# Kernel tuning notes

Measured on AMD Instinct MI355X. Metric: run time of the kernel, lower is better.

The kernel has to match this reference:

```python
import jax, jax.numpy as jnp
import numpy as np
import math

DIM = 384
HEADS = 6
HEAD_DIM = DIM // HEADS
MLP_HIDDEN = int(DIM * 2.0)


def layer_norm(x, g, b, eps=1e-5):
    mu = jnp.mean(x, axis=-1, keepdims=True)
    var = jnp.mean((x - mu) ** 2, axis=-1, keepdims=True)
    return (x - mu) * jax.lax.rsqrt(var + eps) * g + b


def setup_inputs() -> dict:
    key = jax.random.key(0)
    ks = jax.random.split(key, 12)
    B, N = 4, 2048
    s = 0.02
    return {
        "x": jax.random.normal(ks[0], (B, N, DIM), dtype=jnp.float32),
        "pos": jax.random.normal(ks[1], (B, N, 3), dtype=jnp.float32),
        "qkv_w": jax.random.normal(ks[2], (DIM, 3 * DIM), dtype=jnp.float32) * s,
        "qkv_b": jnp.zeros((3 * DIM,), jnp.float32),
        "proj_w": jax.random.normal(ks[3], (DIM, DIM), dtype=jnp.float32) * s,
        "proj_b": jnp.zeros((DIM,), jnp.float32),
        "mlp_w1": jax.random.normal(ks[4], (DIM, MLP_HIDDEN), dtype=jnp.float32) * s,
        "mlp_b1": jnp.zeros((MLP_HIDDEN,), jnp.float32),
        "mlp_w2": jax.random.normal(ks[5], (MLP_HIDDEN, DIM), dtype=jnp.float32) * s,
        "mlp_b2": jnp.zeros((DIM,), jnp.float32),
        "ln1_g": jnp.ones((DIM,), jnp.float32),
        "ln1_b": jnp.zeros((DIM,), jnp.float32),
        "ln2_g": jnp.ones((DIM,), jnp.float32),
        "ln2_b": jnp.zeros((DIM,), jnp.float32),
    }


def reference(x, pos, qkv_w, qkv_b, proj_w, proj_b, mlp_w1, mlp_b1,
              mlp_w2, mlp_b2, ln1_g, ln1_b, ln2_g, ln2_b):
    B, N, D = x.shape
    H, Hd = HEADS, HEAD_DIM
    # qkv projection
    qkv = layer_norm(x, ln1_g, ln1_b) @ qkv_w + qkv_b          # [B,N,3D]
    qkv = qkv.reshape(B, N, 3, H, Hd)
    q = jnp.transpose(qkv[:, :, 0], (0, 2, 1, 3))               # [B,H,N,Hd]
    k = jnp.transpose(qkv[:, :, 1], (0, 2, 1, 3))
    v = jnp.transpose(qkv[:, :, 2], (0, 2, 1, 3))
    # pairwise squared-distance bias: exp(-||p_i - p_j||^2)
    rel = pos[:, :, None, :] - pos[:, None, :, :]               # [B,N,N,3]
    dist = jnp.exp(-jnp.sum(rel ** 2, axis=-1))                 # [B,N,N]
    scale = 1.0 / math.sqrt(Hd)
    attn = jnp.einsum('bhqd,bhkd->bhqk', q, k) * scale + dist[:, None, :, :]
    attn = jax.nn.softmax(attn, axis=-1)
    out = jnp.einsum('bhqk,bhkd->bhqd', attn, v)                # [B,H,N,Hd]
    out = jnp.transpose(out, (0, 2, 1, 3)).reshape(B, N, D)
    out = out @ proj_w + proj_b
    x = x + out
    h = layer_norm(x, ln2_g, ln2_b)
    h = jax.nn.gelu(h @ mlp_w1 + mlp_b1, approximate=False) @ mlp_w2 + mlp_b2
    return x + h
```

## Files before the change

### kernel.cpp

```cpp
#include <hip/hip_runtime.h>
#include <hip/hip_bf16.h>
#include <math.h>

#define DIMD 384
#define NHEADS 6
#define HD 64
#define MLPH 768
#define SEQ 2048
#define NBATCH 4
#define NTOK (NBATCH*SEQ)

typedef __hip_bfloat16 bf16;

typedef __attribute__((ext_vector_type(8))) short bf16x8;
typedef __attribute__((ext_vector_type(4))) float f32x4;

#define LOG2E 1.44269504088896340736f

static __device__ inline float fexp2(float x) { return __builtin_amdgcn_exp2f(x); }

static __device__ inline f32x4 mfma16(bf16x8 a, bf16x8 b, f32x4 c) {
    return __builtin_amdgcn_mfma_f32_16x16x32_bf16(a, b, c, 0, 0, 0);
}

static __device__ inline unsigned int cvtpk(float lo, float hi) {
    unsigned int r;
    asm("v_cvt_pk_bf16_f32 %0, %1, %2" : "=v"(r) : "v"(lo), "v"(hi));
    return r;
}
static __device__ inline float bflo(unsigned int u) { return __builtin_bit_cast(float, u << 16); }
static __device__ inline float bfhi(unsigned int u) { return __builtin_bit_cast(float, u & 0xffff0000u); }

static __device__ inline void gld16(const void* g, void* l) {
    __builtin_amdgcn_global_load_lds(
        (const __attribute__((address_space(1))) unsigned int*)g,
        (__attribute__((address_space(3))) unsigned int*)l, 16, 0, 0);
}

__global__ __launch_bounds__(256) void ln_k(const float* __restrict__ x,
                                            const float* __restrict__ gm,
                                            const float* __restrict__ bt,
                                            bf16* __restrict__ out) {
    int row = blockIdx.x * 4 + (threadIdx.x >> 6);
    int l = threadIdx.x & 63;
    const float* xr = x + (size_t)row * DIMD;
    float v[6];
#pragma unroll
    for (int j = 0; j < 6; ++j) v[j] = xr[l + 64 * j];
    float s = 0.f, s2 = 0.f;
#pragma unroll
    for (int j = 0; j < 6; ++j) { s += v[j]; s2 += v[j] * v[j]; }
#pragma unroll
    for (int m = 1; m < 64; m <<= 1) { s += __shfl_xor(s, m); s2 += __shfl_xor(s2, m); }
    float mu = s * (1.f / DIMD);
    float var = s2 * (1.f / DIMD) - mu * mu;
    float rs = rsqrtf(var + 1e-5f);
    bf16* orow = out + (size_t)row * DIMD;
#pragma unroll
    for (int j = 0; j < 6; ++j) {
        int i = l + 64 * j;
        orow[i] = __float2bfloat16((v[j] - mu) * rs * gm[i] + bt[i]);
    }
}

__global__ __launch_bounds__(256) void wtransall_k(const float* __restrict__ w1,
                                                   const float* __restrict__ w2,
                                                   const float* __restrict__ w3,
                                                   const float* __restrict__ w4,
                                                   bf16* __restrict__ o1,
                                                   bf16* __restrict__ o2,
                                                   bf16* __restrict__ o3,
                                                   bf16* __restrict__ o4) {
    __shared__ float t[32][33];
    int id = blockIdx.x;
    const float* W; bf16* O; int K, N;
    if (id < 432)      { W = w1; O = o1; K = 384; N = 1152; }
    else if (id < 576) { W = w2; O = o2; K = 384; N = 384;  id -= 432; }
    else if (id < 864) { W = w3; O = o3; K = 384; N = 768;  id -= 576; }
    else               { W = w4; O = o4; K = 768; N = 384;  id -= 864; }
    int nbx = N >> 5;
    int nb = (id % nbx) * 32, kb = (id / nbx) * 32;
    int tx = threadIdx.x & 31, ty = threadIdx.x >> 5;
#pragma unroll
    for (int i = 0; i < 4; ++i)
        t[ty + 8 * i][tx] = W[(size_t)(kb + ty + 8 * i) * N + nb + tx];
    __syncthreads();
#pragma unroll
    for (int i = 0; i < 4; ++i)
        O[(size_t)(nb + ty + 8 * i) * K + kb + tx] = __float2bfloat16(t[tx][ty + 8 * i]);
}

__global__ __launch_bounds__(256) void vtrans_k(const bf16* __restrict__ v_,
                                                bf16* __restrict__ vT_) {
    const unsigned short* v = (const unsigned short*)v_;
    unsigned short* vT = (unsigned short*)vT_;
    __shared__ unsigned short t[32][33];
    int tx = threadIdx.x & 31, ty = threadIdx.x >> 5;
    int nb = blockIdx.x * 32, db = blockIdx.y * 32;
    int bh = blockIdx.z;
    const unsigned short* src = v + (size_t)bh * SEQ * HD;
#pragma unroll
    for (int i = 0; i < 4; ++i)
        t[ty + 8 * i][tx] = src[(size_t)(nb + ty + 8 * i) * HD + db + tx];
    __syncthreads();
    unsigned short* dst = vT + (size_t)bh * HD * SEQ;
    int pc = 8 * ((tx & 15) >> 2) + 4 * (tx >> 4) + (tx & 3);
#pragma unroll
    for (int i = 0; i < 4; ++i)
        dst[(size_t)(db + ty + 8 * i) * SEQ + nb + pc] = t[tx][ty + 8 * i];
}

__global__ __launch_bounds__(256) void dist_k(const float* __restrict__ pos,
                                              bf16* __restrict__ DP) {
    int blk = blockIdx.x;
    int w = blk & 3, qt = (blk >> 2) & 31, b = blk >> 7;
    int l = threadIdx.x & 63, tt = threadIdx.x >> 6;
    int lq = l & 15, g = l >> 4;
    int q = qt * 64 + w * 16 + lq;
    const float* pq = pos + ((size_t)b * SEQ + q) * 3;
    float px = pq[0], py = pq[1], pz = pq[2];
    const float* posb = pos + (size_t)b * SEQ * 3;
    char* base = (char*)DP + (size_t)blk * 65536;
    for (int j = 0; j < 8; ++j) {
        int t = tt * 8 + j;
#pragma unroll
        for (int m = 0; m < 2; ++m) {
            int k0 = t * 64 + 32 * m + 4 * g;
            float a[24];
            const float* pk = posb + 3 * k0;
            *(f32x4*)&a[0]  = *(const f32x4*)pk;
            *(f32x4*)&a[4]  = *(const f32x4*)(pk + 4);
            *(f32x4*)&a[8]  = *(const f32x4*)(pk + 8);
            const float* pk2 = posb + 3 * (k0 + 16);
            *(f32x4*)&a[12] = *(const f32x4*)pk2;
            *(f32x4*)&a[16] = *(const f32x4*)(pk2 + 4);
            *(f32x4*)&a[20] = *(const f32x4*)(pk2 + 8);
            float o8[8];
#pragma unroll
            for (int r = 0; r < 8; ++r) {
                float dx = px - a[3 * r], dy = py - a[3 * r + 1], dz = pz - a[3 * r + 2];
                o8[r] = fexp2(-LOG2E * (dx * dx + dy * dy + dz * dz)) * LOG2E;
            }
            uint4 o;
            o.x = cvtpk(o8[0], o8[1]); o.y = cvtpk(o8[2], o8[3]);
            o.z = cvtpk(o8[4], o8[5]); o.w = cvtpk(o8[6], o8[7]);
            *(uint4*)(base + ((size_t)t * 2 + m) * 1024 + l * 16) = o;
        }
    }
}

template <int EPI>
__global__ __launch_bounds__(256) void gemm128_k(const bf16* __restrict__ A,
                                                 const bf16* __restrict__ WT,
                                                 const float* __restrict__ bias,
                                                 bf16* __restrict__ ob0,
                                                 bf16* __restrict__ ob1,
                                                 bf16* __restrict__ ob2,
                                                 int K, int Nw) {
    __shared__ __align__(16) char Als[2][8192];
    __shared__ __align__(16) char Bls[2][8192];
    int tid = threadIdx.x;
    int w = tid >> 6, l = tid & 63;
    int c = l & 15, g = l >> 4;
    int wr = w >> 1, wc = w & 1;
    int m0 = blockIdx.y * 128, n0 = blockIdx.x * 128;
    const char* Ag = (const char*)A + (size_t)m0 * K * 2;
    const char* Bg = (const char*)WT + (size_t)n0 * K * 2;
    int K2 = K * 2;

    f32x4 acc[4][4];
#pragma unroll
    for (int mi = 0; mi < 4; ++mi)
#pragma unroll
        for (int ni = 0; ni < 4; ++ni) acc[mi][ni] = (f32x4){0.f, 0.f, 0.f, 0.f};

    auto stage = [&](int t, int bi) {
#pragma unroll
        for (int p = 0; p < 2; ++p) {
            int chunk = p * 256 + tid;
            int r = chunk >> 2;
            int cc = ((chunk & 3) ^ (r & 3)) << 4;
            gld16(Ag + (size_t)r * K2 + t * 64 + cc, &Als[bi][chunk * 16]);
            gld16(Bg + (size_t)r * K2 + t * 64 + cc, &Bls[bi][chunk * 16]);
        }
    };

    stage(0, 0);
    int kcn = K >> 5;
    for (int t = 0; t < kcn; ++t) {
        int bi = t & 1;
        __syncthreads();
        if (t + 1 < kcn) stage(t + 1, bi ^ 1);
        bf16x8 af[4], bfr[4];
#pragma unroll
        for (int mi = 0; mi < 4; ++mi) {
            int row = wr * 64 + mi * 16 + c;
            __builtin_memcpy(&af[mi], &Als[bi][row * 64 + ((g ^ (row & 3)) << 4)], 16);
        }
#pragma unroll
        for (int ni = 0; ni < 4; ++ni) {
            int row = wc * 64 + ni * 16 + c;
            __builtin_memcpy(&bfr[ni], &Bls[bi][row * 64 + ((g ^ (row & 3)) << 4)], 16);
        }
#pragma unroll
        for (int mi = 0; mi < 4; ++mi)
#pragma unroll
            for (int ni = 0; ni < 4; ++ni)
                acc[mi][ni] = mfma16(af[mi], bfr[ni], acc[mi][ni]);
    }

#pragma unroll
    for (int mi = 0; mi < 4; ++mi) {
#pragma unroll
        for (int ni = 0; ni < 4; ++ni) {
            int ntb = n0 + wc * 64 + ni * 16;
#pragma unroll
            for (int r = 0; r < 4; ++r) {
                int m = m0 + wr * 64 + mi * 16 + 4 * g + r;
                int n = ntb + c;
                float val = acc[mi][ni][r] + bias[n];
                if (EPI == 0) {
                    int which = ntb / DIMD;
                    int rem = ntb - which * DIMD;
                    int h = rem >> 6;
                    int d = (rem & 63) + c;
                    int b = m >> 11, s = m & (SEQ - 1);
                    bf16* dp = which == 0 ? ob0 : (which == 1 ? ob1 : ob2);
                    dp[(((size_t)b * NHEADS + h) * SEQ + s) * HD + d] = __float2bfloat16(val);
                } else {
                    float ge = 0.5f * val * (1.0f + erff(val * 0.70710678118654752f));
                    ob0[(size_t)m * Nw + n] = __float2bfloat16(ge);
                }
            }
        }
    }
}

template <int EPI>
__global__ __launch_bounds__(256) void gemm_k(const bf16* __restrict__ A,
                                              const bf16* __restrict__ WT,
                                              const float* __restrict__ bias,
                                              const float* __restrict__ resid,
                                              float* __restrict__ outf,
                                              int K, int Nw) {
    __shared__ __align__(16) char Als[2][8192];
    __shared__ __align__(16) char Bls[2][8192];
    int tid = threadIdx.x;
    int w = tid >> 6, l = tid & 63;
    int c = l & 15, g = l >> 4;
    int m0 = blockIdx.y * 64, n0 = blockIdx.x * 64;
    const char* Ag = (const char*)A + (size_t)m0 * K * 2;
    const char* Bg = (const char*)WT + (size_t)n0 * K * 2;
    int K2 = K * 2;

    f32x4 acc[4];
#pragma unroll
    for (int nt = 0; nt < 4; ++nt) acc[nt] = (f32x4){0.f, 0.f, 0.f, 0.f};

    auto stage = [&](int t, int bi) {
#pragma unroll
        for (int p = 0; p < 2; ++p) {
            int chunk = p * 256 + tid;
            int r = chunk >> 3;
            int cc = ((chunk & 7) ^ (r & 7)) << 4;
            gld16(Ag + (size_t)r * K2 + t * 128 + cc, &Als[bi][chunk * 16]);
            gld16(Bg + (size_t)r * K2 + t * 128 + cc, &Bls[bi][chunk * 16]);
        }
    };

    stage(0, 0);
    int kcn = K >> 6;
    int arow = (16 * w + c) * 128;
    int sw = c & 7;
    for (int t = 0; t < kcn; ++t) {
        int bi = t & 1;
        __syncthreads();
        if (t + 1 < kcn) stage(t + 1, bi ^ 1);
#pragma unroll
        for (int kk = 0; kk < 2; ++kk) {
            int ch = ((kk * 4 + g) ^ sw) << 4;
            bf16x8 af;
            __builtin_memcpy(&af, &Als[bi][arow + ch], 16);
#pragma unroll
            for (int nt = 0; nt < 4; ++nt) {
                bf16x8 bfr;
                __builtin_memcpy(&bfr, &Bls[bi][(nt * 16 + c) * 128 + ch], 16);
                acc[nt] = mfma16(af, bfr, acc[nt]);
            }
        }
    }

#pragma unroll
    for (int nt = 0; nt < 4; ++nt) {
        int ntb = n0 + nt * 16;
#pragma unroll
        for (int r = 0; r < 4; ++r) {
            int m = m0 + 16 * w + 4 * g + r;
            int n = ntb + c;
            float val = acc[nt][r] + bias[n];
            val += resid[(size_t)m * Nw + n];
            outf[(size_t)m * Nw + n] = val;
        }
    }
}

__global__ __launch_bounds__(256) void attn_k(const bf16* __restrict__ q,
                                              const bf16* __restrict__ k,
                                              const bf16* __restrict__ vT,
                                              const bf16* __restrict__ DP,
                                              bf16* __restrict__ out) {
    __shared__ __align__(16) char Kls[2][8192];
    __shared__ __align__(16) char Vls[2][8192];

    int tid = threadIdx.x;
    int w = tid >> 6, l = tid & 63;
    int lq = l & 15, g = l >> 4;
    int qt = blockIdx.x & 31;
    int bh = blockIdx.x >> 5;
    int b = bh / NHEADS, h = bh % NHEADS;
    int qrow = qt * 64 + w * 16 + lq;

    const bf16* qp = q + ((size_t)bh * SEQ + qrow) * HD + 8 * g;
    bf16x8 qf0 = *(const bf16x8*)qp;
    bf16x8 qf1 = *(const bf16x8*)(qp + 32);

    const char* kgb = (const char*)(k + (size_t)bh * SEQ * HD);
    const char* vgb = (const char*)(vT + (size_t)bh * HD * SEQ);
    const char* dpb = (const char*)DP + ((size_t)((b * 32 + qt) * 4 + w)) * 65536 + l * 16;

    const float SC2 = 0.125f * LOG2E;
    float lloc = 0.f;
    f32x4 oacc[4];
#pragma unroll
    for (int dt = 0; dt < 4; ++dt) oacc[dt] = (f32x4){0.f, 0.f, 0.f, 0.f};

    auto stage = [&](int t, int bi) {
#pragma unroll
        for (int p = 0; p < 2; ++p) {
            int chunk = p * 256 + tid;
            int r = chunk >> 3, c = chunk & 7;
            int cc = (c ^ (r & 7)) << 4;
            gld16(kgb + (size_t)t * 8192 + r * 128 + cc, &Kls[bi][chunk * 16]);
            gld16(vgb + (size_t)r * 4096 + t * 128 + cc, &Vls[bi][chunk * 16]);
        }
    };

    stage(0, 0);
    uint4 cdp0 = *(const uint4*)(dpb);
    uint4 cdp1 = *(const uint4*)(dpb + 1024);

    int swq = lq & 7;
    for (int t = 0; t < 32; ++t) {
        int bi = t & 1;
        __syncthreads();
        uint4 ndp0 = {0, 0, 0, 0}, ndp1 = {0, 0, 0, 0};
        if (t + 1 < 32) {
            stage(t + 1, bi ^ 1);
            const char* dpn = dpb + (size_t)(t + 1) * 2048;
            ndp0 = *(const uint4*)(dpn);
            ndp1 = *(const uint4*)(dpn + 1024);
        }

        f32x4 st[4];
#pragma unroll
        for (int s = 0; s < 4; ++s) {
            int ro = (16 * s + lq) * 128;
            bf16x8 klo, khi;
            __builtin_memcpy(&klo, &Kls[bi][ro + ((g ^ swq) << 4)], 16);
            __builtin_memcpy(&khi, &Kls[bi][ro + (((4 + g) ^ swq) << 4)], 16);
            f32x4 z = (f32x4){0.f, 0.f, 0.f, 0.f};
            st[s] = mfma16(klo, qf0, z);
            st[s] = mfma16(khi, qf1, st[s]);
        }

#pragma unroll
        for (int m = 0; m < 2; ++m) {
            uint4 cd = m == 0 ? cdp0 : cdp1;
            f32x4 s0v = st[2 * m], s1v = st[2 * m + 1];
            float p[8];
            p[0] = fexp2(s0v[0] * SC2 + bflo(cd.x));
            p[1] = fexp2(s0v[1] * SC2 + bfhi(cd.x));
            p[2] = fexp2(s0v[2] * SC2 + bflo(cd.y));
            p[3] = fexp2(s0v[3] * SC2 + bfhi(cd.y));
            p[4] = fexp2(s1v[0] * SC2 + bflo(cd.z));
            p[5] = fexp2(s1v[1] * SC2 + bfhi(cd.z));
            p[6] = fexp2(s1v[2] * SC2 + bflo(cd.w));
            p[7] = fexp2(s1v[3] * SC2 + bfhi(cd.w));
#pragma unroll
            for (int i = 0; i < 8; ++i) lloc += p[i];

            unsigned int pw[4];
            pw[0] = cvtpk(p[0], p[1]);
            pw[1] = cvtpk(p[2], p[3]);
            pw[2] = cvtpk(p[4], p[5]);
            pw[3] = cvtpk(p[6], p[7]);
            bf16x8 pf;
            __builtin_memcpy(&pf, pw, 16);

#pragma unroll
            for (int dt = 0; dt < 4; ++dt) {
                int rv = (16 * dt + lq) * 128;
                bf16x8 vf;
                __builtin_memcpy(&vf, &Vls[bi][rv + (((4 * m + g) ^ swq) << 4)], 16);
                oacc[dt] = mfma16(vf, pf, oacc[dt]);
            }
        }
        cdp0 = ndp0; cdp1 = ndp1;
    }

    float lrun = lloc;
    lrun += __shfl_xor(lrun, 16);
    lrun += __shfl_xor(lrun, 32);
    float inv = 1.f / lrun;
    bf16* op = out + ((size_t)b * SEQ + qrow) * DIMD + h * HD + 4 * g;
#pragma unroll
    for (int dt = 0; dt < 4; ++dt) {
        unsigned int t2[2];
        t2[0] = cvtpk(oacc[dt][0] * inv, oacc[dt][1] * inv);
        t2[1] = cvtpk(oacc[dt][2] * inv, oacc[dt][3] * inv);
        __builtin_memcpy(op + dt * 16, t2, 8);
    }
}

extern "C" void kernel_launch(void* const* d_in, const int* in_sizes, int n_in,
                              void* d_out, int out_size, void* d_ws, size_t ws_size,
                              hipStream_t stream) {
    const float* x      = (const float*)d_in[0];
    const float* pos    = (const float*)d_in[1];
    const float* qkv_w  = (const float*)d_in[2];
    const float* qkv_b  = (const float*)d_in[3];
    const float* proj_w = (const float*)d_in[4];
    const float* proj_b = (const float*)d_in[5];
    const float* mlp_w1 = (const float*)d_in[6];
    const float* mlp_b1 = (const float*)d_in[7];
    const float* mlp_w2 = (const float*)d_in[8];
    const float* mlp_b2 = (const float*)d_in[9];
    const float* ln1_g  = (const float*)d_in[10];
    const float* ln1_b  = (const float*)d_in[11];
    const float* ln2_g  = (const float*)d_in[12];
    const float* ln2_b  = (const float*)d_in[13];

    char* p = (char*)d_ws;
    size_t off = 0;
    auto alloc = [&](size_t bytes) {
        char* r = p + off;
        off = (off + bytes + 255) & ~(size_t)255;
        return r;
    };
    bf16* WT1 = (bf16*)alloc((size_t)1152 * 384 * 2);
    bf16* WT2 = (bf16*)alloc((size_t)384 * 384 * 2);
    bf16* WT3 = (bf16*)alloc((size_t)384 * 768 * 2);
    bf16* WT4 = (bf16*)alloc((size_t)768 * 384 * 2);
    bf16* xn  = (bf16*)alloc((size_t)NTOK * DIMD * 2);
    bf16* xn2 = (bf16*)alloc((size_t)NTOK * DIMD * 2);
    bf16* qb  = (bf16*)alloc((size_t)NTOK * DIMD * 2);
    bf16* kb  = (bf16*)alloc((size_t)NTOK * DIMD * 2);
    bf16* vb  = (bf16*)alloc((size_t)NTOK * DIMD * 2);
    bf16* vTb = (bf16*)alloc((size_t)NTOK * DIMD * 2);
    bf16* ao  = (bf16*)alloc((size_t)NTOK * DIMD * 2);
    float* x1 = (float*)alloc((size_t)NTOK * DIMD * 4);
    bf16* hh  = (bf16*)alloc((size_t)NTOK * MLPH * 2);
    bf16* dtab = (bf16*)alloc((size_t)NBATCH * SEQ * SEQ * 2);
    if (off > ws_size) return;

    wtransall_k<<<1152, 256, 0, stream>>>(qkv_w, proj_w, mlp_w1, mlp_w2,
                                          WT1, WT2, WT3, WT4);

    dist_k<<<NBATCH * 32 * 4, 256, 0, stream>>>(pos, dtab);

    ln_k<<<NTOK / 4, 256, 0, stream>>>(x, ln1_g, ln1_b, xn);
    gemm128_k<0><<<dim3(1152 / 128, NTOK / 128), 256, 0, stream>>>(
        xn, WT1, qkv_b, qb, kb, vb, 384, 1152);
    vtrans_k<<<dim3(SEQ / 32, HD / 32, NBATCH * NHEADS), 256, 0, stream>>>(vb, vTb);
    attn_k<<<NBATCH * NHEADS * (SEQ / 64), 256, 0, stream>>>(qb, kb, vTb, dtab, ao);
    gemm_k<1><<<dim3(384 / 64, NTOK / 64), 256, 0, stream>>>(
        ao, WT2, proj_b, x, x1, 384, 384);
    ln_k<<<NTOK / 4, 256, 0, stream>>>(x1, ln2_g, ln2_b, xn2);
    gemm128_k<2><<<dim3(768 / 128, NTOK / 128), 256, 0, stream>>>(
        xn2, WT3, mlp_b1, hh, nullptr, nullptr, 384, 768);
    gemm_k<3><<<dim3(384 / 64, NTOK / 64), 256, 0, stream>>>(
        hh, WT4, mlp_b2, x1, (float*)d_out, 768, 384);
}
```

Measured before the change: 144.3 us.

## Merge prep kernels, fuse V transpose into QKV GEMM, triple-buffer attention loop

Combines weight transpose, distance-table generation and the first layernorm into one prep kernel, which removes two launches. The QKV GEMM epilogue now writes V directly in the permuted transposed layout, so the separate V-transpose kernel and its buffer are gone. The attention loop moves from double to triple buffering, using explicit waitcnt, barriers and priority hints. It also computes the softmax row sum with an MFMA against a ones vector in place of per-lane adds and shuffles. This uses more LDS per block, which may lower occupancy, and the epilogue writes to V are scattered.

```diff
diff --git a/kernel.cpp b/kernel.cpp
--- a/kernel.cpp
+++ b/kernel.cpp
@@ -63,88 +63,94 @@
     }
 }
 
-__global__ __launch_bounds__(256) void wtransall_k(const float* __restrict__ w1,
-                                                   const float* __restrict__ w2,
-                                                   const float* __restrict__ w3,
-                                                   const float* __restrict__ w4,
-                                                   bf16* __restrict__ o1,
-                                                   bf16* __restrict__ o2,
-                                                   bf16* __restrict__ o3,
-                                                   bf16* __restrict__ o4) {
+__global__ __launch_bounds__(256) void prep_k(const float* __restrict__ w1,
+                                              const float* __restrict__ w2,
+                                              const float* __restrict__ w3,
+                                              const float* __restrict__ w4,
+                                              bf16* __restrict__ o1,
+                                              bf16* __restrict__ o2,
+                                              bf16* __restrict__ o3,
+                                              bf16* __restrict__ o4,
+                                              const float* __restrict__ pos,
+                                              bf16* __restrict__ DP,
+                                              const float* __restrict__ x,
+                                              const float* __restrict__ g1,
+                                              const float* __restrict__ b1,
+                                              bf16* __restrict__ xn) {
     __shared__ float t[32][33];
     int id = blockIdx.x;
-    const float* W; bf16* O; int K, N;
-    if (id < 432)      { W = w1; O = o1; K = 384; N = 1152; }
-    else if (id < 576) { W = w2; O = o2; K = 384; N = 384;  id -= 432; }
-    else if (id < 864) { W = w3; O = o3; K = 384; N = 768;  id -= 576; }
-    else               { W = w4; O = o4; K = 768; N = 384;  id -= 864; }
-    int nbx = N >> 5;
-    int nb = (id % nbx) * 32, kb = (id / nbx) * 32;
-    int tx = threadIdx.x & 31, ty = threadIdx.x >> 5;
-#pragma unroll
-    for (int i = 0; i < 4; ++i)
-        t[ty + 8 * i][tx] = W[(size_t)(kb + ty + 8 * i) * N + nb + tx];
-    __syncthreads();
-#pragma unroll
-    for (int i = 0; i < 4; ++i)
-        O[(size_t)(nb + ty + 8 * i) * K + kb + tx] = __float2bfloat16(t[tx][ty + 8 * i]);
-}
-
-__global__ __launch_bounds__(256) void vtrans_k(const bf16* __restrict__ v_,
-                                                bf16* __restrict__ vT_) {
-    const unsigned short* v = (const unsigned short*)v_;
-    unsigned short* vT = (unsigned short*)vT_;
-    __shared__ unsigned short t[32][33];
-    int tx = threadIdx.x & 31, ty = threadIdx.x >> 5;
-    int nb = blockIdx.x * 32, db = blockIdx.y * 32;
-    int bh = blockIdx.z;
-    const unsigned short* src = v + (size_t)bh * SEQ * HD;
-#pragma unroll
-    for (int i = 0; i < 4; ++i)
-        t[ty + 8 * i][tx] = src[(size_t)(nb + ty + 8 * i) * HD + db + tx];
-    __syncthreads();
-    unsigned short* dst = vT + (size_t)bh * HD * SEQ;
-    int pc = 8 * ((tx & 15) >> 2) + 4 * (tx >> 4) + (tx & 3);
-#pragma unroll
-    for (int i = 0; i < 4; ++i)
-        dst[(size_t)(db + ty + 8 * i) * SEQ + nb + pc] = t[tx][ty + 8 * i];
-}
-
-__global__ __launch_bounds__(256) void dist_k(const float* __restrict__ pos,
-                                              bf16* __restrict__ DP) {
-    int blk = blockIdx.x;
-    int w = blk & 3, qt = (blk >> 2) & 31, b = blk >> 7;
-    int l = threadIdx.x & 63, tt = threadIdx.x >> 6;
-    int lq = l & 15, g = l >> 4;
-    int q = qt * 64 + w * 16 + lq;
-    const float* pq = pos + ((size_t)b * SEQ + q) * 3;
-    float px = pq[0], py = pq[1], pz = pq[2];
-    const float* posb = pos + (size_t)b * SEQ * 3;
-    char* base = (char*)DP + (size_t)blk * 65536;
-    for (int j = 0; j < 8; ++j) {
-        int t = tt * 8 + j;
-#pragma unroll
-        for (int m = 0; m < 2; ++m) {
-            int k0 = t * 64 + 32 * m + 4 * g;
-            float a[24];
-            const float* pk = posb + 3 * k0;
-            *(f32x4*)&a[0]  = *(const f32x4*)pk;
-            *(f32x4*)&a[4]  = *(const f32x4*)(pk + 4);
-            *(f32x4*)&a[8]  = *(const f32x4*)(pk + 8);
-            const float* pk2 = posb + 3 * (k0 + 16);
-            *(f32x4*)&a[12] = *(const f32x4*)pk2;
-            *(f32x4*)&a[16] = *(const f32x4*)(pk2 + 4);
-            *(f32x4*)&a[20] = *(const f32x4*)(pk2 + 8);
-            float o8[8];
-#pragma unroll
-            for (int r = 0; r < 8; ++r) {
-                float dx = px - a[3 * r], dy = py - a[3 * r + 1], dz = pz - a[3 * r + 2];
-                o8[r] = fexp2(-LOG2E * (dx * dx + dy * dy + dz * dz)) * LOG2E;
+    if (id < 1152) {
+        const float* W; bf16* O; int K, N;
+        if (id < 432)      { W = w1; O = o1; K = 384; N = 1152; }
+        else if (id < 576) { W = w2; O = o2; K = 384; N = 384;  id -= 432; }
+        else if (id < 864) { W = w3; O = o3; K = 384; N = 768;  id -= 576; }
+        else               { W = w4; O = o4; K = 768; N = 384;  id -= 864; }
+        int nbx = N >> 5;
+        int nb = (id % nbx) * 32, kb = (id / nbx) * 32;
+        int tx = threadIdx.x & 31, ty = threadIdx.x >> 5;
+#pragma unroll
+        for (int i = 0; i < 4; ++i)
+            t[ty + 8 * i][tx] = W[(size_t)(kb + ty + 8 * i) * N + nb + tx];
+        __syncthreads();
+#pragma unroll
+        for (int i = 0; i < 4; ++i)
+            O[(size_t)(nb + ty + 8 * i) * K + kb + tx] = __float2bfloat16(t[tx][ty + 8 * i]);
+    } else if (id < 1664) {
+        int blk = id - 1152;
+        int w = blk & 3, qt = (blk >> 2) & 31, b = blk >> 7;
+        int l = threadIdx.x & 63, tt = threadIdx.x >> 6;
+        int lq = l & 15, g = l >> 4;
+        int q = qt * 64 + w * 16 + lq;
+        const float* pq = pos + ((size_t)b * SEQ + q) * 3;
+        float px = pq[0], py = pq[1], pz = pq[2];
+        const float* posb = pos + (size_t)b * SEQ * 3;
+        char* base = (char*)DP + (size_t)blk * 65536;
+        for (int j = 0; j < 8; ++j) {
+            int tt8 = tt * 8 + j;
+#pragma unroll
+            for (int m = 0; m < 2; ++m) {
+                int k0 = tt8 * 64 + 32 * m + 4 * g;
+                float a[24];
+                const float* pk = posb + 3 * k0;
+                *(f32x4*)&a[0]  = *(const f32x4*)pk;
+                *(f32x4*)&a[4]  = *(const f32x4*)(pk + 4);
+                *(f32x4*)&a[8]  = *(const f32x4*)(pk + 8);
+                const float* pk2 = posb + 3 * (k0 + 16);
+                *(f32x4*)&a[12] = *(const f32x4*)pk2;
+                *(f32x4*)&a[16] = *(const f32x4*)(pk2 + 4);
+                *(f32x4*)&a[20] = *(const f32x4*)(pk2 + 8);
+                float o8[8];
+#pragma unroll
+                for (int r = 0; r < 8; ++r) {
+                    float dx = px - a[3 * r], dy = py - a[3 * r + 1], dz = pz - a[3 * r + 2];
+                    o8[r] = fexp2(-LOG2E * (dx * dx + dy * dy + dz * dz)) * LOG2E;
+                }
+                uint4 o;
+                o.x = cvtpk(o8[0], o8[1]); o.y = cvtpk(o8[2], o8[3]);
+                o.z = cvtpk(o8[4], o8[5]); o.w = cvtpk(o8[6], o8[7]);
+                *(uint4*)(base + ((size_t)tt8 * 2 + m) * 1024 + l * 16) = o;
             }
-            uint4 o;
-            o.x = cvtpk(o8[0], o8[1]); o.y = cvtpk(o8[2], o8[3]);
-            o.z = cvtpk(o8[4], o8[5]); o.w = cvtpk(o8[6], o8[7]);
-            *(uint4*)(base + ((size_t)t * 2 + m) * 1024 + l * 16) = o;
+        }
+    } else {
+        int row = (id - 1664) * 4 + (threadIdx.x >> 6);
+        int l = threadIdx.x & 63;
+        const float* xr = x + (size_t)row * DIMD;
+        float v[6];
+#pragma unroll
+        for (int j = 0; j < 6; ++j) v[j] = xr[l + 64 * j];
+        float s = 0.f, s2 = 0.f;
+#pragma unroll
+        for (int j = 0; j < 6; ++j) { s += v[j]; s2 += v[j] * v[j]; }
+#pragma unroll
+        for (int m = 1; m < 64; m <<= 1) { s += __shfl_xor(s, m); s2 += __shfl_xor(s2, m); }
+        float mu = s * (1.f / DIMD);
+        float var = s2 * (1.f / DIMD) - mu * mu;
+        float rs = rsqrtf(var + 1e-5f);
+        bf16* orow = xn + (size_t)row * DIMD;
+#pragma unroll
+        for (int j = 0; j < 6; ++j) {
+            int i = l + 64 * j;
+            orow[i] = __float2bfloat16((v[j] - mu) * rs * g1[i] + b1[i]);
         }
     }
 }
@@ -225,8 +231,13 @@
                     int h = rem >> 6;
                     int d = (rem & 63) + c;
                     int b = m >> 11, s = m & (SEQ - 1);
-                    bf16* dp = which == 0 ? ob0 : (which == 1 ? ob1 : ob2);
-                    dp[(((size_t)b * NHEADS + h) * SEQ + s) * HD + d] = __float2bfloat16(val);
+                    if (which == 2) {
+                        int slot = (s & ~31) + 8 * ((m & 15) >> 2) + 4 * ((m >> 4) & 1) + (m & 3);
+                        ob2[(((size_t)b * NHEADS + h) * HD + d) * SEQ + slot] = __float2bfloat16(val);
+                    } else {
+                        bf16* dp = which == 0 ? ob0 : ob1;
+                        dp[(((size_t)b * NHEADS + h) * SEQ + s) * HD + d] = __float2bfloat16(val);
+                    }
                 } else {
                     float ge = 0.5f * val * (1.0f + erff(val * 0.70710678118654752f));
                     ob0[(size_t)m * Nw + n] = __float2bfloat16(ge);
@@ -309,8 +320,8 @@
                                               const bf16* __restrict__ vT,
                                               const bf16* __restrict__ DP,
                                               bf16* __restrict__ out) {
-    __shared__ __align__(16) char Kls[2][8192];
-    __shared__ __align__(16) char Vls[2][8192];
+    __shared__ __align__(16) char Kls[3][8192];
+    __shared__ __align__(16) char Vls[3][8192];
 
     int tid = threadIdx.x;
     int w = tid >> 6, l = tid & 63;
@@ -329,10 +340,12 @@
     const char* dpb = (const char*)DP + ((size_t)((b * 32 + qt) * 4 + w)) * 65536 + l * 16;
 
     const float SC2 = 0.125f * LOG2E;
-    float lloc = 0.f;
     f32x4 oacc[4];
 #pragma unroll
     for (int dt = 0; dt < 4; ++dt) oacc[dt] = (f32x4){0.f, 0.f, 0.f, 0.f};
+    f32x4 osum = (f32x4){0.f, 0.f, 0.f, 0.f};
+    bf16x8 ones = {(short)0x3F80, (short)0x3F80, (short)0x3F80, (short)0x3F80,
+                   (short)0x3F80, (short)0x3F80, (short)0x3F80, (short)0x3F80};
 
     auto stage = [&](int t, int bi) {
 #pragma unroll
@@ -348,30 +361,29 @@
     stage(0, 0);
     uint4 cdp0 = *(const uint4*)(dpb);
     uint4 cdp1 = *(const uint4*)(dpb + 1024);
-
+    stage(1, 1);
+
+    int ib0 = 0, ib1 = 1, ib2 = 2;
     int swq = lq & 7;
     for (int t = 0; t < 32; ++t) {
-        int bi = t & 1;
-        __syncthreads();
-        uint4 ndp0 = {0, 0, 0, 0}, ndp1 = {0, 0, 0, 0};
-        if (t + 1 < 32) {
-            stage(t + 1, bi ^ 1);
-            const char* dpn = dpb + (size_t)(t + 1) * 2048;
-            ndp0 = *(const uint4*)(dpn);
-            ndp1 = *(const uint4*)(dpn + 1024);
-        }
+        asm volatile("s_waitcnt vmcnt(4)" ::: "memory");
+        __builtin_amdgcn_sched_barrier(0);
+        __builtin_amdgcn_s_barrier();
+        __builtin_amdgcn_sched_barrier(0);
 
         f32x4 st[4];
+        __builtin_amdgcn_s_setprio(1);
 #pragma unroll
         for (int s = 0; s < 4; ++s) {
             int ro = (16 * s + lq) * 128;
             bf16x8 klo, khi;
-            __builtin_memcpy(&klo, &Kls[bi][ro + ((g ^ swq) << 4)], 16);
-            __builtin_memcpy(&khi, &Kls[bi][ro + (((4 + g) ^ swq) << 4)], 16);
+            __builtin_memcpy(&klo, &Kls[ib0][ro + ((g ^ swq) << 4)], 16);
+            __builtin_memcpy(&khi, &Kls[ib0][ro + (((4 + g) ^ swq) << 4)], 16);
             f32x4 z = (f32x4){0.f, 0.f, 0.f, 0.f};
             st[s] = mfma16(klo, qf0, z);
             st[s] = mfma16(khi, qf1, st[s]);
         }
+        __builtin_amdgcn_s_setprio(0);
 
 #pragma unroll
         for (int m = 0; m < 2; ++m) {
@@ -386,8 +398,6 @@
             p[5] = fexp2(s1v[1] * SC2 + bfhi(cd.z));
             p[6] = fexp2(s1v[2] * SC2 + bflo(cd.w));
             p[7] = fexp2(s1v[3] * SC2 + bfhi(cd.w));
-#pragma unroll
-            for (int i = 0; i < 8; ++i) lloc += p[i];
 
             unsigned int pw[4];
             pw[0] = cvtpk(p[0], p[1]);
@@ -397,21 +407,32 @@
             bf16x8 pf;
             __builtin_memcpy(&pf, pw, 16);
 
+            __builtin_amdgcn_s_setprio(1);
+            osum = mfma16(ones, pf, osum);
 #pragma unroll
             for (int dt = 0; dt < 4; ++dt) {
                 int rv = (16 * dt + lq) * 128;
                 bf16x8 vf;
-                __builtin_memcpy(&vf, &Vls[bi][rv + (((4 * m + g) ^ swq) << 4)], 16);
+                __builtin_memcpy(&vf, &Vls[ib0][rv + (((4 * m + g) ^ swq) << 4)], 16);
                 oacc[dt] = mfma16(vf, pf, oacc[dt]);
             }
-        }
+            __builtin_amdgcn_s_setprio(0);
+        }
+
+        __builtin_amdgcn_sched_barrier(0);
+        int tn1 = t + 1 < 32 ? t + 1 : 31;
+        const char* dpn = dpb + (size_t)tn1 * 2048;
+        uint4 ndp0 = *(const uint4*)(dpn);
+        uint4 ndp1 = *(const uint4*)(dpn + 1024);
+        __builtin_amdgcn_sched_barrier(0);
+        int tn2 = t + 2 < 32 ? t + 2 : 31;
+        stage(tn2, ib2);
+        __builtin_amdgcn_sched_barrier(0);
         cdp0 = ndp0; cdp1 = ndp1;
-    }
-
-    float lrun = lloc;
-    lrun += __shfl_xor(lrun, 16);
-    lrun += __shfl_xor(lrun, 32);
-    float inv = 1.f / lrun;
+        int tmp = ib0; ib0 = ib1; ib1 = ib2; ib2 = tmp;
+    }
+
+    float inv = 1.f / osum[0];
     bf16* op = out + ((size_t)b * SEQ + qrow) * DIMD + h * HD + 4 * g;
 #pragma unroll
     for (int dt = 0; dt < 4; ++dt) {
@@ -455,7 +476,6 @@
     bf16* xn2 = (bf16*)alloc((size_t)NTOK * DIMD * 2);
     bf16* qb  = (bf16*)alloc((size_t)NTOK * DIMD * 2);
     bf16* kb  = (bf16*)alloc((size_t)NTOK * DIMD * 2);
-    bf16* vb  = (bf16*)alloc((size_t)NTOK * DIMD * 2);
     bf16* vTb = (bf16*)alloc((size_t)NTOK * DIMD * 2);
     bf16* ao  = (bf16*)alloc((size_t)NTOK * DIMD * 2);
     float* x1 = (float*)alloc((size_t)NTOK * DIMD * 4);
@@ -463,15 +483,12 @@
     bf16* dtab = (bf16*)alloc((size_t)NBATCH * SEQ * SEQ * 2);
     if (off > ws_size) return;
 
-    wtransall_k<<<1152, 256, 0, stream>>>(qkv_w, proj_w, mlp_w1, mlp_w2,
-                                          WT1, WT2, WT3, WT4);
-
-    dist_k<<<NBATCH * 32 * 4, 256, 0, stream>>>(pos, dtab);
-
-    ln_k<<<NTOK / 4, 256, 0, stream>>>(x, ln1_g, ln1_b, xn);
+    prep_k<<<1152 + 512 + 2048, 256, 0, stream>>>(
+        qkv_w, proj_w, mlp_w1, mlp_w2, WT1, WT2, WT3, WT4,
+        pos, dtab, x, ln1_g, ln1_b, xn);
+
     gemm128_k<0><<<dim3(1152 / 128, NTOK / 128), 256, 0, stream>>>(
-        xn, WT1, qkv_b, qb, kb, vb, 384, 1152);
-    vtrans_k<<<dim3(SEQ / 32, HD / 32, NBATCH * NHEADS), 256, 0, stream>>>(vb, vTb);
+        xn, WT1, qkv_b, qb, kb, vTb, 384, 1152);
     attn_k<<<NBATCH * NHEADS * (SEQ / 64), 256, 0, stream>>>(qb, kb, vTb, dtab, ao);
     gemm_k<1><<<dim3(384 / 64, NTOK / 64), 256, 0, stream>>>(
         ao, WT2, proj_b, x, x1, 384, 384);
```

Result: no change. 141.8 us (-1.7%).
